# Performance work log

Hardware: AMD Instinct MI355X
Metric: run time of the kernel (lower is better)

The kernel has to match this reference:

```python
import jax, jax.numpy as jnp
import numpy as np

WINDOW = 2  # hardcoded global in the original module


def band_count(seq_len, window=WINDOW):
    """C[a,b] = number of positions i whose local window covers both a and b.
    Windows (from converse_qk): i=0 -> [0, W]; i=1 -> [0, W+1];
    i=seq-2 -> [seq-W-2, seq-1]; i=seq-1 -> [seq-W-1, seq-1]; else [i-W, i+W].
    """
    i = jnp.arange(seq_len)
    lo = jnp.clip(i - window, 0, None)
    hi = jnp.clip(i + window, None, seq_len - 1)
    lo = jnp.where(i == 1, 0, lo)
    hi = jnp.where(i == 1, window + 1, hi)
    lo = jnp.where(i == seq_len - 2, seq_len - window - 2, lo)
    hi = jnp.where(i == seq_len - 2, seq_len - 1, hi)
    a = jnp.arange(seq_len)[None, :]
    M = ((a >= lo[:, None]) & (a <= hi[:, None])).astype(jnp.float32)  # [i, a]
    return M.T @ M  # [seq, seq]


def setup_inputs() -> dict:
    key = jax.random.key(0)
    ks = jax.random.split(key, 12)
    bs, seq, d_model = 2, 2048, 512
    s = 1.0 / np.sqrt(d_model)
    inp = {
        'q': jax.random.normal(ks[0], (bs, seq, d_model), jnp.float32),
        'k': jax.random.normal(ks[1], (bs, seq, d_model), jnp.float32),
        'v': jax.random.normal(ks[2], (bs, seq, d_model), jnp.float32),
        'Wq': jax.random.normal(ks[3], (d_model, d_model), jnp.float32) * s,
        'bq': jnp.zeros((d_model,), jnp.float32),
        'Wk': jax.random.normal(ks[4], (d_model, d_model), jnp.float32) * s,
        'bk': jnp.zeros((d_model,), jnp.float32),
        'Wv': jax.random.normal(ks[5], (d_model, d_model), jnp.float32) * s,
        'bv': jnp.zeros((d_model,), jnp.float32),
        'Wo': jax.random.normal(ks[6], (d_model, d_model), jnp.float32) * s,
        'bo': jnp.zeros((d_model,), jnp.float32),
    }
    return inp


def reference(q, k, v, Wq, bq, Wk, bk, Wv, bv, Wo, bo):
    bs, seq, d_model = q.shape
    heads = 8
    d_k = d_model // heads
    # projections (torch Linear uses x @ W.T + b; here W stored already transposed)
    qh = (q @ Wq + bq).reshape(bs, seq, heads, d_k).transpose(0, 2, 1, 3)
    kh = (k @ Wk + bk).reshape(bs, seq, heads, d_k).transpose(0, 2, 1, 3)
    vh = (v @ Wv + bv).reshape(bs, seq, heads, d_k).transpose(0, 2, 1, 3)
    C = band_count(seq)  # [seq, seq] window-overlap counts
    scores = jnp.einsum('bhqd,bhkd->bhqk', qh, kh) / jnp.sqrt(jnp.float32(d_k))
    scores = scores * C  # banded count-weighted scores; zeros outside band
    attn = jax.nn.softmax(scores, axis=-1)  # full-row softmax, as in original
    out = jnp.einsum('bhqk,bhkd->bhqd', attn, vh)
    concat = out.transpose(0, 2, 1, 3).reshape(bs, seq, d_model)
    return concat @ Wo + bo
```

## Files before the change

### kernel.cpp

```cpp
#include <hip/hip_runtime.h>
#include <hip/hip_bf16.h>

#define SEQ 2048
#define DM  512
#define BS  2
#define NH  8
#define DK  64
#define MROWS (BS * SEQ)
#define GK 64

typedef __attribute__((ext_vector_type(8))) short bf16x8;
typedef __attribute__((ext_vector_type(4))) float f32x4;

__device__ __forceinline__ unsigned short f2bf(float f) {
    unsigned int u = __float_as_uint(f);
    u += 0x7fff + ((u >> 16) & 1);
    return (unsigned short)(u >> 16);
}

#define GLDS16(g, l) __builtin_amdgcn_global_load_lds( \
    (const __attribute__((address_space(1))) void*)(g), \
    (__attribute__((address_space(3))) void*)(unsigned int)(unsigned long long)(l), 16, 0, 0)

__global__ __launch_bounds__(256) void prep_kernel(const float* __restrict__ q,
                                                   const float* __restrict__ k,
                                                   const float* __restrict__ v,
                                                   const float* __restrict__ Wq, const float* __restrict__ Wk,
                                                   const float* __restrict__ Wv, const float* __restrict__ Wo,
                                                   const float* __restrict__ bv_,
                                                   unsigned short* __restrict__ qb,
                                                   unsigned short* __restrict__ kb,
                                                   unsigned short* __restrict__ vb,
                                                   unsigned short* __restrict__ WqT, unsigned short* __restrict__ WkT,
                                                   unsigned short* __restrict__ WvT, unsigned short* __restrict__ WoT,
                                                   float* __restrict__ vsum)
{
    __shared__ float tile[32][33];
    const int bid = blockIdx.x;
    if (bid == 0) {
        #pragma unroll
        for (int t = 0; t < 4; ++t) {
            const int idx = threadIdx.x * 4 + t;
            vsum[idx] = (float)SEQ * bv_[idx & (DM - 1)];
        }
    }
    if (bid < 3072) {
        const int z = bid >> 10;
        const int blk = bid & 1023;
        const float* src = (z == 0) ? q : (z == 1) ? k : v;
        unsigned short* dst = (z == 0) ? qb : (z == 1) ? kb : vb;
        const size_t idx = ((size_t)blk * 256 + threadIdx.x) * 8;
        float4 v0 = *(const float4*)(src + idx);
        float4 v1 = *(const float4*)(src + idx + 4);
        ushort4 o0, o1;
        o0.x = f2bf(v0.x); o0.y = f2bf(v0.y); o0.z = f2bf(v0.z); o0.w = f2bf(v0.w);
        o1.x = f2bf(v1.x); o1.y = f2bf(v1.y); o1.z = f2bf(v1.z); o1.w = f2bf(v1.w);
        *(ushort4*)(dst + idx) = o0;
        *(ushort4*)(dst + idx + 4) = o1;
    } else {
        const int t = bid - 3072;
        const int z = t >> 8;
        const int tl = t & 255;
        const float* W = (z == 0) ? Wq : (z == 1) ? Wk : (z == 2) ? Wv : Wo;
        unsigned short* T = (z == 0) ? WqT : (z == 1) ? WkT : (z == 2) ? WvT : WoT;
        const int n0 = (tl & 15) * 32, k0 = (tl >> 4) * 32;
        const int tx = threadIdx.x & 31;
        const int ty = threadIdx.x >> 5;
        #pragma unroll
        for (int r = 0; r < 32; r += 8)
            tile[ty + r][tx] = W[(size_t)(k0 + ty + r) * DM + n0 + tx];
        __syncthreads();
        #pragma unroll
        for (int r = 0; r < 32; r += 8)
            T[(size_t)(n0 + ty + r) * DM + k0 + tx] = f2bf(tile[tx][ty + r]);
    }
}

template<int TGM, int TGN, int WMT, int WNT>
__device__ __forceinline__ void gemm_core(const unsigned short* __restrict__ A,
                                          const unsigned short* __restrict__ BT,
                                          const float* __restrict__ bias,
                                          float* __restrict__ C,
                                          float* __restrict__ vsumP)
{
    __shared__ unsigned short S[(TGM + TGN) * GK];

    const int tid  = threadIdx.x;
    const int lane = tid & 63;
    const int wave = tid >> 6;
    constexpr int WAVES_M = TGM / (WMT * 16);
    const int wm = (wave % WAVES_M) * (WMT * 16);
    const int wn = (wave / WAVES_M) * (WNT * 16);
    const int m0 = blockIdx.y * TGM;
    const int n0 = blockIdx.x * TGN;
    const int l15 = lane & 15;
    const int q8  = (lane >> 4) * 8;

    f32x4 acc[WMT][WNT];
    #pragma unroll
    for (int i = 0; i < WMT; ++i)
        #pragma unroll
        for (int j = 0; j < WNT; ++j)
            acc[i][j] = (f32x4){0.f, 0.f, 0.f, 0.f};

    constexpr int NCH = (TGM + TGN) * 8;
    constexpr int NIT = NCH / 256;
    const unsigned short* gp[NIT];
    unsigned short* lp[NIT];
    #pragma unroll
    for (int it = 0; it < NIT; ++it) {
        const int c = tid + it * 256;
        if (c < TGM * 8) {
            const int kk = c / (TGM * 4);
            const int cr = c - kk * (TGM * 4);
            gp[it] = A + (size_t)(m0 + (cr >> 2)) * DM + kk * 32 + (cr & 3) * 8;
        } else {
            const int cb = c - TGM * 8;
            const int kk = cb / (TGN * 4);
            const int cr = cb - kk * (TGN * 4);
            gp[it] = BT + (size_t)(n0 + (cr >> 2)) * DM + kk * 32 + (cr & 3) * 8;
        }
        lp[it] = &S[(size_t)c * 8];
    }

    for (int k0 = 0; k0 < DM; k0 += GK) {
        #pragma unroll
        for (int it = 0; it < NIT; ++it)
            GLDS16(gp[it] + k0, lp[it]);
        __syncthreads();

        #pragma unroll
        for (int kk = 0; kk < 2; ++kk) {
            bf16x8 af[WMT], bfr[WNT];
            #pragma unroll
            for (int i = 0; i < WMT; ++i)
                af[i] = *(const bf16x8*)&S[kk * TGM * 32 + (wm + i * 16 + l15) * 32 + q8];
            #pragma unroll
            for (int j = 0; j < WNT; ++j)
                bfr[j] = *(const bf16x8*)&S[TGM * 64 + kk * TGN * 32 + (wn + j * 16 + l15) * 32 + q8];
            #pragma unroll
            for (int i = 0; i < WMT; ++i)
                #pragma unroll
                for (int j = 0; j < WNT; ++j)
                    acc[i][j] = __builtin_amdgcn_mfma_f32_16x16x32_bf16(af[i], bfr[j], acc[i][j], 0, 0, 0);
        }
        __syncthreads();
    }

    #pragma unroll
    for (int j = 0; j < WNT; ++j) {
        const int col = n0 + wn + j * 16 + l15;
        const float bv = bias[col];
        #pragma unroll
        for (int i = 0; i < WMT; ++i) {
            const int rbase = m0 + wm + i * 16 + (lane >> 4) * 4;
            #pragma unroll
            for (int r = 0; r < 4; ++r)
                C[(size_t)(rbase + r) * DM + col] = acc[i][j][r] + bv;
        }
    }

    if (vsumP) {
        const int b = m0 >> 11;
        #pragma unroll
        for (int j = 0; j < WNT; ++j) {
            float part = 0.f;
            #pragma unroll
            for (int i = 0; i < WMT; ++i)
                #pragma unroll
                for (int r = 0; r < 4; ++r)
                    part += acc[i][j][r];
            part += __shfl_xor(part, 16, 64);
            part += __shfl_xor(part, 32, 64);
            if ((lane >> 4) == 0)
                atomicAdd(&vsumP[b * DM + wn + n0 + j * 16 + l15], part);
        }
    }
}

__global__ __launch_bounds__(256) void gemm_qkv(const unsigned short* qb, const unsigned short* kb, const unsigned short* vb,
                                                const unsigned short* WqT, const unsigned short* WkT, const unsigned short* WvT,
                                                const float* bq, const float* bk, const float* bv,
                                                float* Qp, float* Kp, float* Vp, float* vsum)
{
    const unsigned short* A;  const unsigned short* BT;  const float* bias;  float* C;  float* vs;
    if (blockIdx.z == 0)      { A = qb; BT = WqT; bias = bq; C = Qp; vs = nullptr; }
    else if (blockIdx.z == 1) { A = kb; BT = WkT; bias = bk; C = Kp; vs = nullptr; }
    else                      { A = vb; BT = WvT; bias = bv; C = Vp; vs = vsum; }
    gemm_core<128, 64, 4, 2>(A, BT, bias, C, vs);
}

__global__ __launch_bounds__(256) void gemm_out(const unsigned short* A, const unsigned short* BT,
                                                const float* bias, float* C)
{
    gemm_core<64, 64, 2, 2>(A, BT, bias, C, nullptr);
}

__global__ __launch_bounds__(256) void attn_kernel(const float* __restrict__ Qp,
                                                   const float* __restrict__ Kp,
                                                   const float* __restrict__ Vp,
                                                   const float* __restrict__ vsum,
                                                   unsigned short* __restrict__ concat)
{
    const int d = threadIdx.x;
    const int qpos = blockIdx.x * 4 + threadIdx.y;
    const int h = blockIdx.y & 7;
    const int b = blockIdx.y >> 3;
    const int col = h * DK + d;
    const size_t rowbase = (size_t)b * SEQ;
    const float* Kcol = Kp + rowbase * DM + col;
    const float* Vcol = Vp + rowbase * DM + col;

    const float qd = Qp[(rowbase + qpos) * DM + col];
    float acc = vsum[b * DM + col];
    float den = (float)SEQ;

    float p[9], vv[9], cw[9];
    #pragma unroll
    for (int j = 0; j < 9; ++j) {
        const int k = qpos - 4 + j;
        const int kc = min(max(k, 0), SEQ - 1);
        p[j]  = qd * Kcol[(size_t)kc * DM];
        vv[j] = Vcol[(size_t)kc * DM];
        const int mn = min(qpos, k);
        const int mx = qpos + k - mn;
        const float cnt = (float)(min(mn + 2, SEQ - 1) - max(mx - 2, 0) + 1);
        cw[j] = (k >= 0 && k < SEQ) ? cnt * 0.125f : 0.0f;
    }
    #pragma unroll
    for (int off = 32; off >= 1; off >>= 1)
        #pragma unroll
        for (int j = 0; j < 9; ++j)
            p[j] += __shfl_xor(p[j], off, 64);
    #pragma unroll
    for (int j = 0; j < 9; ++j) {
        const float w = expf(p[j] * cw[j]) - 1.0f;
        acc += w * vv[j];
        den += w;
    }
    concat[(rowbase + qpos) * DM + col] = f2bf(acc / den);
}

extern "C" void kernel_launch(void* const* d_in, const int* in_sizes, int n_in,
                              void* d_out, int out_size, void* d_ws, size_t ws_size,
                              hipStream_t stream) {
    const float* q  = (const float*)d_in[0];
    const float* k  = (const float*)d_in[1];
    const float* v  = (const float*)d_in[2];
    const float* Wq = (const float*)d_in[3];
    const float* bq = (const float*)d_in[4];
    const float* Wk = (const float*)d_in[5];
    const float* bk = (const float*)d_in[6];
    const float* Wv = (const float*)d_in[7];
    const float* bv = (const float*)d_in[8];
    const float* Wo = (const float*)d_in[9];
    const float* bo = (const float*)d_in[10];

    const size_t NE = (size_t)MROWS * DM;

    float* ws = (float*)d_ws;
    float* Qp   = ws;
    float* Kp   = Qp + NE;
    float* Vp   = Kp + NE;
    float* vsum = Vp + NE;
    unsigned short* qb     = (unsigned short*)(vsum + 1024);
    unsigned short* kb     = qb + NE;
    unsigned short* vb     = kb + NE;
    unsigned short* WqT    = vb + NE;
    unsigned short* WkT    = WqT + DM * DM;
    unsigned short* WvT    = WkT + DM * DM;
    unsigned short* WoT    = WvT + DM * DM;
    unsigned short* concat = WoT + DM * DM;

    prep_kernel<<<4096, 256, 0, stream>>>(q, k, v, Wq, Wk, Wv, Wo, bv,
                                          qb, kb, vb, WqT, WkT, WvT, WoT, vsum);

    gemm_qkv<<<dim3(DM / 64, MROWS / 128, 3), 256, 0, stream>>>(qb, kb, vb, WqT, WkT, WvT,
                                                                bq, bk, bv, Qp, Kp, Vp, vsum);

    attn_kernel<<<dim3(SEQ / 4, BS * NH), dim3(64, 4), 0, stream>>>(Qp, Kp, Vp, vsum, concat);

    gemm_out<<<dim3(DM / 64, MROWS / 64), 256, 0, stream>>>(concat, WoT, bo, (float*)d_out);
}
```

Measured before the change: 137.1 us.

## Store QKV projections as bf16 and compute banded attention with MFMA

The QKV projection GEMM now writes bf16 outputs instead of fp32, which halves the intermediate traffic. The per-query scalar attention kernel, which did shuffle reductions over nine neighbours, is replaced by a one-wave-per-16-queries kernel. That kernel computes a 16x32 score tile with MFMA, stages the bf16 weights in LDS, and does the weight-times-V product with another MFMA. The cost is lower precision for Q/K/V and for the attention weights, and V is gathered with strided scalar loads.

```diff
diff --git a/kernel.cpp b/kernel.cpp
--- a/kernel.cpp
+++ b/kernel.cpp
@@ -16,6 +16,9 @@
     unsigned int u = __float_as_uint(f);
     u += 0x7fff + ((u >> 16) & 1);
     return (unsigned short)(u >> 16);
+}
+__device__ __forceinline__ float bf2f(unsigned short b) {
+    return __uint_as_float((unsigned int)b << 16);
 }
 
 #define GLDS16(g, l) __builtin_amdgcn_global_load_lds( \
@@ -76,11 +79,11 @@
     }
 }
 
-template<int TGM, int TGN, int WMT, int WNT>
+template<int TGM, int TGN, int WMT, int WNT, bool BF16OUT>
 __device__ __forceinline__ void gemm_core(const unsigned short* __restrict__ A,
                                           const unsigned short* __restrict__ BT,
                                           const float* __restrict__ bias,
-                                          float* __restrict__ C,
+                                          void* __restrict__ Cv,
                                           float* __restrict__ vsumP)
 {
     __shared__ unsigned short S[(TGM + TGN) * GK];
@@ -155,8 +158,13 @@
         for (int i = 0; i < WMT; ++i) {
             const int rbase = m0 + wm + i * 16 + (lane >> 4) * 4;
             #pragma unroll
-            for (int r = 0; r < 4; ++r)
-                C[(size_t)(rbase + r) * DM + col] = acc[i][j][r] + bv;
+            for (int r = 0; r < 4; ++r) {
+                const float val = acc[i][j][r] + bv;
+                if (BF16OUT)
+                    ((unsigned short*)Cv)[(size_t)(rbase + r) * DM + col] = f2bf(val);
+                else
+                    ((float*)Cv)[(size_t)(rbase + r) * DM + col] = val;
+            }
         }
     }
 
@@ -181,64 +189,98 @@
 __global__ __launch_bounds__(256) void gemm_qkv(const unsigned short* qb, const unsigned short* kb, const unsigned short* vb,
                                                 const unsigned short* WqT, const unsigned short* WkT, const unsigned short* WvT,
                                                 const float* bq, const float* bk, const float* bv,
-                                                float* Qp, float* Kp, float* Vp, float* vsum)
-{
-    const unsigned short* A;  const unsigned short* BT;  const float* bias;  float* C;  float* vs;
-    if (blockIdx.z == 0)      { A = qb; BT = WqT; bias = bq; C = Qp; vs = nullptr; }
-    else if (blockIdx.z == 1) { A = kb; BT = WkT; bias = bk; C = Kp; vs = nullptr; }
-    else                      { A = vb; BT = WvT; bias = bv; C = Vp; vs = vsum; }
-    gemm_core<128, 64, 4, 2>(A, BT, bias, C, vs);
+                                                unsigned short* Qb, unsigned short* Kb, unsigned short* Vb, float* vsum)
+{
+    const unsigned short* A;  const unsigned short* BT;  const float* bias;  unsigned short* C;  float* vs;
+    if (blockIdx.z == 0)      { A = qb; BT = WqT; bias = bq; C = Qb; vs = nullptr; }
+    else if (blockIdx.z == 1) { A = kb; BT = WkT; bias = bk; C = Kb; vs = nullptr; }
+    else                      { A = vb; BT = WvT; bias = bv; C = Vb; vs = vsum; }
+    gemm_core<128, 64, 4, 2, true>(A, BT, bias, C, vs);
 }
 
 __global__ __launch_bounds__(256) void gemm_out(const unsigned short* A, const unsigned short* BT,
                                                 const float* bias, float* C)
 {
-    gemm_core<64, 64, 2, 2>(A, BT, bias, C, nullptr);
-}
-
-__global__ __launch_bounds__(256) void attn_kernel(const float* __restrict__ Qp,
-                                                   const float* __restrict__ Kp,
-                                                   const float* __restrict__ Vp,
-                                                   const float* __restrict__ vsum,
-                                                   unsigned short* __restrict__ concat)
-{
-    const int d = threadIdx.x;
-    const int qpos = blockIdx.x * 4 + threadIdx.y;
-    const int h = blockIdx.y & 7;
-    const int b = blockIdx.y >> 3;
-    const int col = h * DK + d;
+    gemm_core<64, 64, 2, 2, false>(A, BT, bias, C, nullptr);
+}
+
+__global__ __launch_bounds__(64) void attn_mfma(const unsigned short* __restrict__ Qb,
+                                                const unsigned short* __restrict__ Kb,
+                                                const unsigned short* __restrict__ Vb,
+                                                const float* __restrict__ vsum,
+                                                unsigned short* __restrict__ concat)
+{
+    __shared__ unsigned short Wlds[16 * 32];
+    const int lane = threadIdx.x;
+    const int l15  = lane & 15;
+    const int quad = lane >> 4;
+    const int bh = blockIdx.y;
+    const int b = bh >> 3, h = bh & 7;
+    const int q0 = blockIdx.x * 16;
     const size_t rowbase = (size_t)b * SEQ;
-    const float* Kcol = Kp + rowbase * DM + col;
-    const float* Vcol = Vp + rowbase * DM + col;
-
-    const float qd = Qp[(rowbase + qpos) * DM + col];
-    float acc = vsum[b * DM + col];
-    float den = (float)SEQ;
-
-    float p[9], vv[9], cw[9];
-    #pragma unroll
-    for (int j = 0; j < 9; ++j) {
-        const int k = qpos - 4 + j;
-        const int kc = min(max(k, 0), SEQ - 1);
-        p[j]  = qd * Kcol[(size_t)kc * DM];
-        vv[j] = Vcol[(size_t)kc * DM];
-        const int mn = min(qpos, k);
-        const int mx = qpos + k - mn;
-        const float cnt = (float)(min(mn + 2, SEQ - 1) - max(mx - 2, 0) + 1);
-        cw[j] = (k >= 0 && k < SEQ) ? cnt * 0.125f : 0.0f;
-    }
-    #pragma unroll
-    for (int off = 32; off >= 1; off >>= 1)
-        #pragma unroll
-        for (int j = 0; j < 9; ++j)
-            p[j] += __shfl_xor(p[j], off, 64);
-    #pragma unroll
-    for (int j = 0; j < 9; ++j) {
-        const float w = expf(p[j] * cw[j]) - 1.0f;
-        acc += w * vv[j];
-        den += w;
-    }
-    concat[(rowbase + qpos) * DM + col] = f2bf(acc / den);
+    const int dbase = h * DK;
+
+    const unsigned short* qrow = Qb + (rowbase + q0 + l15) * DM + dbase + quad * 8;
+    const bf16x8 aq0 = *(const bf16x8*)(qrow);
+    const bf16x8 aq1 = *(const bf16x8*)(qrow + 32);
+
+    f32x4 sc[2];
+    #pragma unroll
+    for (int t = 0; t < 2; ++t) {
+        int kp = q0 - 4 + t * 16 + l15;
+        kp = min(max(kp, 0), SEQ - 1);
+        const unsigned short* krow = Kb + (rowbase + kp) * DM + dbase + quad * 8;
+        const bf16x8 b0 = *(const bf16x8*)(krow);
+        const bf16x8 b1 = *(const bf16x8*)(krow + 32);
+        f32x4 z = (f32x4){0.f, 0.f, 0.f, 0.f};
+        z = __builtin_amdgcn_mfma_f32_16x16x32_bf16(aq0, b0, z, 0, 0, 0);
+        sc[t] = __builtin_amdgcn_mfma_f32_16x16x32_bf16(aq1, b1, sc[t] = z, 0, 0, 0);
+    }
+
+    float dsum[4] = {0.f, 0.f, 0.f, 0.f};
+    #pragma unroll
+    for (int t = 0; t < 2; ++t) {
+        const int kpos = q0 - 4 + t * 16 + l15;
+        #pragma unroll
+        for (int r = 0; r < 4; ++r) {
+            const int qq = q0 + quad * 4 + r;
+            const int mn = min(qq, kpos), mx = qq + kpos - mn;
+            const float cnt = (float)(min(mn + 2, SEQ - 1) - max(mx - 2, 0) + 1);
+            const float cw = (kpos >= 0 && kpos < SEQ && (mx - mn) <= 4) ? cnt * 0.125f : 0.f;
+            const float w = expf(sc[t][r] * cw) - 1.f;
+            const unsigned short wb = f2bf(w);
+            Wlds[(quad * 4 + r) * 32 + t * 16 + l15] = wb;
+            dsum[r] += bf2f(wb);
+        }
+    }
+    #pragma unroll
+    for (int off = 1; off <= 8; off <<= 1)
+        #pragma unroll
+        for (int r = 0; r < 4; ++r)
+            dsum[r] += __shfl_xor(dsum[r], off, 64);
+
+    __syncthreads();
+    const bf16x8 aw = *(const bf16x8*)&Wlds[l15 * 32 + quad * 8];
+
+    #pragma unroll
+    for (int nt = 0; nt < 4; ++nt) {
+        const int d = dbase + nt * 16 + l15;
+        bf16x8 bv_;
+        #pragma unroll
+        for (int j = 0; j < 8; ++j) {
+            int kr = q0 - 4 + quad * 8 + j;
+            kr = min(max(kr, 0), SEQ - 1);
+            bv_[j] = (short)Vb[(rowbase + kr) * DM + d];
+        }
+        f32x4 z = (f32x4){0.f, 0.f, 0.f, 0.f};
+        const f32x4 o = __builtin_amdgcn_mfma_f32_16x16x32_bf16(aw, bv_, z, 0, 0, 0);
+        const float vs = vsum[b * DM + d];
+        #pragma unroll
+        for (int r = 0; r < 4; ++r) {
+            const float den = (float)SEQ + dsum[r];
+            concat[(rowbase + q0 + quad * 4 + r) * DM + d] = f2bf((vs + o[r]) / den);
+        }
+    }
 }
 
 extern "C" void kernel_launch(void* const* d_in, const int* in_sizes, int n_in,
@@ -258,12 +300,11 @@
 
     const size_t NE = (size_t)MROWS * DM;
 
-    float* ws = (float*)d_ws;
-    float* Qp   = ws;
-    float* Kp   = Qp + NE;
-    float* Vp   = Kp + NE;
-    float* vsum = Vp + NE;
-    unsigned short* qb     = (unsigned short*)(vsum + 1024);
+    float* vsum = (float*)d_ws;
+    unsigned short* Qb     = (unsigned short*)(vsum + 1024);
+    unsigned short* Kb     = Qb + NE;
+    unsigned short* Vb     = Kb + NE;
+    unsigned short* qb     = Vb + NE;
     unsigned short* kb     = qb + NE;
     unsigned short* vb     = kb + NE;
     unsigned short* WqT    = vb + NE;
@@ -276,9 +317,9 @@
                                           qb, kb, vb, WqT, WkT, WvT, WoT, vsum);
 
     gemm_qkv<<<dim3(DM / 64, MROWS / 128, 3), 256, 0, stream>>>(qb, kb, vb, WqT, WkT, WvT,
-                                                                bq, bk, bv, Qp, Kp, Vp, vsum);
-
-    attn_kernel<<<dim3(SEQ / 4, BS * NH), dim3(64, 4), 0, stream>>>(Qp, Kp, Vp, vsum, concat);
+                                                                bq, bk, bv, Qb, Kb, Vb, vsum);
+
+    attn_mfma<<<dim3(SEQ / 16, BS * NH), 64, 0, stream>>>(Qb, Kb, Vb, vsum, concat);
 
     gemm_out<<<dim3(DM / 64, MROWS / 64), 256, 0, stream>>>(concat, WoT, bo, (float*)d_out);
 }
```

Measured after the change: 124.9 us. 8.9% less time.
